# Kernel tuning notes

Measured on AMD Instinct MI355X. Metric: run time of the kernel, lower is better.

## Reference

```python
import jax, jax.numpy as jnp
import numpy as np

N_STEP = 3
N_INP = 256


def setup_inputs() -> dict:
    key = jax.random.key(0)
    ks = jax.random.split(key, 8)
    bs, L, n = 16, 128, N_INP
    s = 1.0 / np.sqrt(n)
    s2 = 1.0 / np.sqrt(2 * n)
    feat = jax.random.normal(ks[0], (bs, L, n), dtype=jnp.float32)
    mask = jnp.ones((bs, L), dtype=jnp.float32)
    # stacked per-step Linear params (torch Linear: y = x @ W.T + b)
    aggW = jax.random.uniform(ks[1], (N_STEP, n, n), minval=-s, maxval=s, dtype=jnp.float32)
    aggB = jax.random.uniform(ks[2], (N_STEP, n), minval=-s, maxval=s, dtype=jnp.float32)
    attnW = jax.random.uniform(ks[3], (N_STEP, n, 2 * n), minval=-s2, maxval=s2, dtype=jnp.float32)
    attnB = jax.random.uniform(ks[4], (N_STEP, n), minval=-s2, maxval=s2, dtype=jnp.float32)
    updW = jax.random.uniform(ks[5], (N_STEP, n, 2 * n), minval=-s2, maxval=s2, dtype=jnp.float32)
    updB = jax.random.uniform(ks[6], (N_STEP, n), minval=-s2, maxval=s2, dtype=jnp.float32)
    return {"feat": feat, "mask": mask, "aggW": aggW, "aggB": aggB,
            "attnW": attnW, "attnB": attnB, "updW": updW, "updB": updB}


def reference(feat, mask, aggW, aggB, attnW, attnB, updW, updB):
    bs, L, n = feat.shape
    hid = feat
    for i in range(N_STEP):
        hid = hid * mask[:, :, None]
        x = hid @ aggW[i].T + aggB[i]  # [b, s, n]
        # attn Linear on concat(x_s, x_j) splits into two matmuls
        W1 = attnW[i][:, :n]   # acts on x_s (sequence position)
        W2 = attnW[i][:, n:]   # acts on x_j (query node)
        p = x @ W1.T           # [b, s, n]
        q = x @ W2.T           # [b, j, n]
        # logits[b, j, s, c] = p[b, s, c] + q[b, j, c] + bias[c]
        logits = p[:, None, :, :] + q[:, :, None, :] + attnB[i]
        w = jax.nn.softmax(logits, axis=2)  # softmax over sequence dim per channel
        agg = jax.nn.sigmoid(jnp.einsum('bjsn,bsn->bjn', w, x))
        cat = jnp.concatenate([x, agg], axis=-1)  # [b, s, 2n]; dropout is identity (eval)
        hid = cat @ updW[i].T + updB[i]
    return hid
```

## Files before the change

kernel.cpp:

```cpp
#include <hip/hip_runtime.h>
#include <hip/hip_fp16.h>

#define NBLK  256
#define NPACK 192
#define NT    512
#define FPAD  16

typedef _Float16 h2_t  __attribute__((ext_vector_type(2)));
typedef _Float16 half8 __attribute__((ext_vector_type(8)));
typedef float    f32x4 __attribute__((ext_vector_type(4)));

#define AG_LD(p)    __hip_atomic_load((p), __ATOMIC_RELAXED, __HIP_MEMORY_SCOPE_AGENT)
#define AG_ST(p, v) __hip_atomic_store((p), (v), __ATOMIC_RELAXED, __HIP_MEMORY_SCOPE_AGENT)

__device__ __forceinline__ unsigned pkh(float a, float b) {
    const __half2 h = __floats2half2_rn(a, b);
    return __builtin_bit_cast(unsigned, h);
}
__device__ __forceinline__ float fdot2(unsigned w, unsigned a, float c) {
#if __has_builtin(__builtin_amdgcn_fdot2)
    return __builtin_amdgcn_fdot2(__builtin_bit_cast(h2_t, w),
                                  __builtin_bit_cast(h2_t, a), c, false);
#else
    const float2 fw = __half22float2(__builtin_bit_cast(__half2, w));
    const float2 fa = __half22float2(__builtin_bit_cast(__half2, a));
    return c + fw.x * fa.x + fw.y * fa.y;
#endif
}

__device__ __forceinline__ half8 ldw(const unsigned* p) {
    return __builtin_bit_cast(half8, *(const uint4*)p);
}
__device__ __forceinline__ f32x4 MF(half8 a, half8 b, f32x4 c) {
    return __builtin_amdgcn_mfma_f32_16x16x32_f16(a, b, c, 0, 0, 0);
}

__device__ __forceinline__ void bar_arrive(int n, unsigned* flags, int lid) {
    __syncthreads();
    if (threadIdx.x == 0)
        __hip_atomic_store(&flags[lid * FPAD], (unsigned)n, __ATOMIC_RELEASE,
                           __HIP_MEMORY_SCOPE_AGENT);
}
__device__ __forceinline__ void bar_wait_batch(int n, unsigned* flags, int b) {
    if (threadIdx.x < 16) {
        while ((int)__hip_atomic_load(&flags[(b * 16 + threadIdx.x) * FPAD],
                                      __ATOMIC_RELAXED,
                                      __HIP_MEMORY_SCOPE_AGENT) < n)
            __builtin_amdgcn_s_sleep(1);
    }
    __syncthreads();
}


__global__ __launch_bounds__(NT, 2) void pack_k(
    const float* __restrict__ aggW, const float* __restrict__ attnW,
    const float* __restrict__ updW, unsigned* __restrict__ WtH,
    unsigned* __restrict__ flags)
{
    __shared__ float Tl[64][65];
    const int bb = blockIdx.x, tid = threadIdx.x;
    const int m = bb >> 4, t = bb & 15, tr = t >> 2, tc = t & 3;
    const float* src; int stride, off;
    if (m < 3)      { src = aggW  + (size_t)m * 65536;        stride = 256; off = 0;   }
    else if (m < 6) { src = attnW + (size_t)(m - 3) * 131072; stride = 512; off = 0;   }
    else if (m < 9) { src = updW  + (size_t)(m - 6) * 131072; stride = 512; off = 0;   }
    else            { src = updW  + (size_t)(m - 9) * 131072; stride = 512; off = 256; }
    unsigned* dstu = WtH + (size_t)m * 32768;
    #pragma unroll
    for (int it = 0; it < 2; ++it) {
        const int j = it * 512 + tid, row = j >> 4, q = (j & 15) * 4;
        const float4 v = *(const float4*)(src + (size_t)(tr * 64 + row) * stride + off + tc * 64 + q);
        Tl[row][q + 0] = v.x; Tl[row][q + 1] = v.y;
        Tl[row][q + 2] = v.z; Tl[row][q + 3] = v.w;
    }
    if (bb == 0)
        for (int z = tid; z < NBLK * FPAD; z += NT) flags[z] = 0u;
    __syncthreads();
    #pragma unroll
    for (int it = 0; it < 4; ++it) {
        const int j = it * 512 + tid, cl = j >> 5, pr = j & 31;
        const unsigned val = pkh(Tl[cl][pr * 2], Tl[cl][pr * 2 + 1]);
        const int C = tr * 64 + cl, P = tc * 32 + pr;
        size_t idx;
        if (m < 9) {
            const int ttn = C >> 4, lc = C & 15;
            const int kc = P >> 4, g = (P >> 2) & 3, sl = P & 3;
            idx = (size_t)((ttn * 8 + kc) * 256 + (g * 16 + lc) * 4 + sl);
        } else {
            idx = (size_t)(P >> 2) * 1024 + (size_t)C * 4 + (P & 3);
        }
        dstu[idx] = val;
    }
}

__device__ __forceinline__ float phaseB(int i, int b, int c, int rq, int tid,
                                        const float* __restrict__ part,
                                        const unsigned* __restrict__ WtH,
                                        const float* __restrict__ updB,
                                        float* S, unsigned* aggh, uint4* buf) {
    const float* pbase = part + (size_t)((i & 1) * 256 + b * 16 + rq * 8) * 768;
    float m[8], d[8], nn[8];
    #pragma unroll
    for (int j = 0; j < 8; ++j) {
        const float* pp = pbase + (size_t)j * 768;
        m[j]  = AG_LD(pp + c);
        d[j]  = AG_LD(pp + 256 + c);
        nn[j] = AG_LD(pp + 512 + c);
    }
    #pragma unroll
    for (int st = 1; st < 8; st <<= 1) {
        #pragma unroll
        for (int j = 0; j < 8; j += 2 * st) {
            const float Mn = fmaxf(m[j], m[j + st]);
            const float sa = __expf(m[j] - Mn), sb = __expf(m[j + st] - Mn);
            d[j]  = d[j] * sa + d[j + st] * sb;
            nn[j] = nn[j] * sa + nn[j + st] * sb;
            m[j]  = Mn;
        }
    }
    S[rq * 256 + c] = m[0];
    S[512 + rq * 256 + c] = d[0];
    S[1024 + rq * 256 + c] = nn[0];
    __syncthreads();
    if (tid < 128) {
        float sg[2];
        #pragma unroll
        for (int u = 0; u < 2; ++u) {
            const int cc = 2 * tid + u;
            const float m0 = S[cc], m1 = S[256 + cc];
            const float Mx = fmaxf(m0, m1);
            const float s0 = __expf(m0 - Mx), s1 = __expf(m1 - Mx);
            const float dd = S[512 + cc] * s0 + S[768 + cc] * s1;
            const float nv = S[1024 + cc] * s0 + S[1280 + cc] * s1;
            sg[u] = 1.f / (1.f + __expf(-(nv / dd)));
        }
        aggh[tid] = pkh(sg[0], sg[1]);
    }
    __syncthreads();
    const unsigned* Uq = WtH + (size_t)(9 + i) * 32768;
    const int g0 = rq * 16;
    float a0 = 0.f, a1 = 0.f, a2 = 0.f, a3 = 0.f;
    #pragma unroll
    for (int ph = 0; ph < 2; ++ph) {
        #pragma unroll
        for (int j = 0; j < 8; ++j) {
            const uint4 w = buf[j];
            if (ph < 1)
                buf[j] = *(const uint4*)(Uq + (size_t)(g0 + 8 + j) * 1024 + c * 4);
            const uint4 a = *(const uint4*)&aggh[(g0 + ph * 8 + j) * 4];
            a0 = fdot2(w.x, a.x, a0);
            a1 = fdot2(w.y, a.y, a1);
            a2 = fdot2(w.z, a.z, a2);
            a3 = fdot2(w.w, a.w, a3);
        }
    }
    const float au = (a0 + a1) + (a2 + a3);
    S[rq * 256 + c] = au;
    __syncthreads();
    return S[c] + S[256 + c] + updB[i * 256 + c];
}

__global__ __launch_bounds__(NT, 2) void main_k(
    const float* __restrict__ feat,
    const float* __restrict__ mask,
    const float* __restrict__ aggB,
    const float* __restrict__ updB,
    const unsigned* __restrict__ WtH,
    float* __restrict__ part,
    unsigned* flags,
    float* __restrict__ out)
{
    __shared__ __align__(16) float ldsf[6152];
    unsigned* hid_uu = (unsigned*)ldsf;
    unsigned* x_uu   = (unsigned*)ldsf + 2112;
    float*    accl   = ldsf + 4224;
    float*    S      = ldsf + 4480;
    unsigned* aggh   = (unsigned*)ldsf + 6016;
    float*    msk    = ldsf + 6144;

    const int bid = blockIdx.x;
    const int tid = threadIdx.x;
    const int c   = tid & 255;
    const int rq  = tid >> 8;
    const int wid = tid >> 6, lane = tid & 63;
    const int lr  = lane & 15, lg = lane >> 4;
    const int b   = 2 * (bid & 7) + ((bid >> 3) & 1);
    const int jj  = bid >> 4;
    const int lid = b * 16 + jj;
    const int row0 = b * 128 + jj * 8;

    #pragma unroll
    for (int it = 0; it < 2; ++it) {
        const int j = it * 512 + tid, r = j >> 7, pr = j & 127;
        const float2 f = *(const float2*)(feat + (size_t)(row0 + r) * 256 + pr * 2);
        const float mv = mask[row0 + r];
        hid_uu[r * 132 + pr] = pkh(f.x * mv, f.y * mv);
    }
    for (int z = tid; z < 1056; z += NT) {
        hid_uu[1056 + z] = 0u;
        x_uu[1056 + z] = 0u;
    }
    if (tid < 8) msk[tid] = mask[row0 + tid];
    __syncthreads();

    f32x4 xu0 = {}, xu1 = {};
    uint4 u2buf[8];

    for (int i = 0; i < 3; ++i) {
        if (i > 0) {
            const float accU = phaseB(i - 1, b, c, rq, tid, part, WtH, updB,
                                      S, aggh, u2buf);
            if (rq == 0) accl[c] = accU;
            __syncthreads();
            #pragma unroll
            for (int tt = 0; tt < 2; ++tt) {
                const int t = wid * 2 + tt;
                const f32x4 xa = tt ? xu1 : xu0;
                const float av = accl[t * 16 + lr];
                float hv[4], pv[4];
                #pragma unroll
                for (int q = 0; q < 4; ++q)
                    hv[q] = (xa[q] + av) * msk[(lg & 1) * 4 + q];
                #pragma unroll
                for (int q = 0; q < 4; ++q) pv[q] = __shfl_xor(hv[q], 1);
                if (lg < 2 && !(lr & 1)) {
                    const int p2 = t * 8 + (lr >> 1);
                    #pragma unroll
                    for (int q = 0; q < 4; ++q)
                        hid_uu[(lg * 4 + q) * 132 + p2] = pkh(hv[q], pv[q]);
                }
            }
            __syncthreads();
        }

        f32x4 xr0, xr1;

        {
            const unsigned* W0 = WtH + (size_t)i * 32768;
            half8 a[8];
            #pragma unroll
            for (int kc = 0; kc < 8; ++kc)
                a[kc] = ldw(hid_uu + lr * 132 + kc * 16 + lg * 4);
            #pragma unroll
            for (int tt = 0; tt < 2; ++tt) {
                const int t = wid * 2 + tt;
                f32x4 acc = {};
                #pragma unroll
                for (int kc = 0; kc < 8; ++kc)
                    acc = MF(a[kc], ldw(W0 + (size_t)(t * 8 + kc) * 256 + lane * 4), acc);
                const float bb = aggB[i * 256 + t * 16 + lr];
                #pragma unroll
                for (int q = 0; q < 4; ++q) acc[q] += bb;
                if (tt) xr1 = acc; else xr0 = acc;
                float pv[4];
                #pragma unroll
                for (int q = 0; q < 4; ++q) pv[q] = __shfl_xor(acc[q], 1);
                if (lg < 2 && !(lr & 1)) {
                    const int p2 = t * 8 + (lr >> 1);
                    #pragma unroll
                    for (int q = 0; q < 4; ++q)
                        x_uu[(lg * 4 + q) * 132 + p2] = pkh(acc[q], pv[q]);
                }
            }
            __syncthreads();
        }

        {
            const unsigned* W1 = WtH + (size_t)(3 + i) * 32768;
            const unsigned* U1 = WtH + (size_t)(6 + i) * 32768;
            half8 a2[8];
            #pragma unroll
            for (int kc = 0; kc < 8; ++kc)
                a2[kc] = ldw(x_uu + lr * 132 + kc * 16 + lg * 4);
            float* pb = part + (size_t)((i & 1) * 256 + lid) * 768;
            #pragma unroll
            for (int tt = 0; tt < 2; ++tt) {
                const int t = wid * 2 + tt;
                f32x4 acc = {};
                #pragma unroll
                for (int kc = 0; kc < 8; ++kc)
                    acc = MF(a2[kc], ldw(W1 + (size_t)(t * 8 + kc) * 256 + lane * 4), acc);
                const f32x4 xa = tt ? xr1 : xr0;
                float m4 = fmaxf(fmaxf(acc[0], acc[1]), fmaxf(acc[2], acc[3]));
                const float m8 = fmaxf(m4, __shfl_xor(m4, 16));
                float d4 = 0.f, n4 = 0.f;
                #pragma unroll
                for (int q = 0; q < 4; ++q) {
                    const float e = __expf(acc[q] - m8);
                    d4 += e;
                    n4 += e * xa[q];
                }
                const float d8 = d4 + __shfl_xor(d4, 16);
                const float n8 = n4 + __shfl_xor(n4, 16);
                if (lg == 0) {
                    const int cc = t * 16 + lr;
                    AG_ST(pb + cc, m8);
                    AG_ST(pb + 256 + cc, d8);
                    AG_ST(pb + 512 + cc, n8);
                }
            }
            bar_arrive(i + 1, flags, lid);
            #pragma unroll
            for (int tt = 0; tt < 2; ++tt) {
                const int t = wid * 2 + tt;
                f32x4 acc = {};
                #pragma unroll
                for (int kc = 0; kc < 8; ++kc)
                    acc = MF(a2[kc], ldw(U1 + (size_t)(t * 8 + kc) * 256 + lane * 4), acc);
                if (tt) xu1 = acc; else xu0 = acc;
            }
            {
                const unsigned* Uq = WtH + (size_t)(9 + i) * 32768;
                #pragma unroll
                for (int j = 0; j < 8; ++j)
                    u2buf[j] = *(const uint4*)(Uq + (size_t)(rq * 16 + j) * 1024 + c * 4);
            }
            bar_wait_batch(i + 1, flags, b);
        }
    }

    {
        const float accU = phaseB(2, b, c, rq, tid, part, WtH, updB, S, aggh, u2buf);
        if (rq == 0) accl[c] = accU;
        __syncthreads();
        #pragma unroll
        for (int tt = 0; tt < 2; ++tt) {
            const int t = wid * 2 + tt;
            const f32x4 xa = tt ? xu1 : xu0;
            const float av = accl[t * 16 + lr];
            if (lg < 2) {
                #pragma unroll
                for (int q = 0; q < 4; ++q)
                    out[(size_t)(row0 + lg * 4 + q) * 256 + t * 16 + lr] = xa[q] + av;
            }
        }
    }
}

extern "C" void kernel_launch(void* const* d_in, const int* in_sizes, int n_in,
                              void* d_out, int out_size, void* d_ws, size_t ws_size,
                              hipStream_t stream) {
    const float* feat  = (const float*)d_in[0];
    const float* mask  = (const float*)d_in[1];
    const float* aggW  = (const float*)d_in[2];
    const float* aggB  = (const float*)d_in[3];
    const float* attnW = (const float*)d_in[4];
    const float* updW  = (const float*)d_in[6];
    const float* updB  = (const float*)d_in[7];

    unsigned* WtH = (unsigned*)d_ws;
    float* part = (float*)(WtH + 12 * 32768);
    unsigned* flags = (unsigned*)(part + 2 * 256 * 768);

    pack_k<<<NPACK, NT, 0, stream>>>(aggW, attnW, updW, WtH, flags);
    main_k<<<NBLK, NT, 0, stream>>>(feat, mask, aggB, updB, WtH, part, flags,
                                    (float*)d_out);
}
```

Before: 109.8 us.

## Software-pipeline weight fragments in registers across consecutive MFMA phases

Adds a 16-entry register buffer of weight fragments, loaded before the main loop. Each MFMA phase consumes the current buffer while prefetching the weights for the next matmul (agg to attn to upd to next step's agg), so global weight latency overlaps with compute. The kernel is also pinned to exactly two waves per EU. This costs 64 extra VGPRs per thread, which risks spills under the occupancy bound, and it issues one wasted prefetch at the last step.

Measured after the change: 115.0 us. 1.05x slower.

```diff
diff --git a/kernel.cpp b/kernel.cpp
--- a/kernel.cpp
+++ b/kernel.cpp
@@ -30,6 +30,9 @@
 
 __device__ __forceinline__ half8 ldw(const unsigned* p) {
     return __builtin_bit_cast(half8, *(const uint4*)p);
+}
+__device__ __forceinline__ half8 h8(uint4 w) {
+    return __builtin_bit_cast(half8, w);
 }
 __device__ __forceinline__ f32x4 MF(half8 a, half8 b, f32x4 c) {
     return __builtin_amdgcn_mfma_f32_16x16x32_f16(a, b, c, 0, 0, 0);
@@ -160,7 +163,9 @@
     return S[c] + S[256 + c] + updB[i * 256 + c];
 }
 
-__global__ __launch_bounds__(NT, 2) void main_k(
+__global__ __launch_bounds__(NT, 2)
+__attribute__((amdgpu_waves_per_eu(2, 2)))
+void main_k(
     const float* __restrict__ feat,
     const float* __restrict__ mask,
     const float* __restrict__ aggB,
@@ -201,6 +206,11 @@
         x_uu[1056 + z] = 0u;
     }
     if (tid < 8) msk[tid] = mask[row0 + tid];
+
+    uint4 wb[16];
+    #pragma unroll
+    for (int j = 0; j < 16; ++j)
+        wb[j] = *(const uint4*)(WtH + (size_t)(wid * 16 + j) * 256 + lane * 4);
     __syncthreads();
 
     f32x4 xu0 = {}, xu1 = {};
@@ -236,7 +246,7 @@
         f32x4 xr0, xr1;
 
         {
-            const unsigned* W0 = WtH + (size_t)i * 32768;
+            const unsigned* W1 = WtH + (size_t)(3 + i) * 32768;
             half8 a[8];
             #pragma unroll
             for (int kc = 0; kc < 8; ++kc)
@@ -246,8 +256,12 @@
                 const int t = wid * 2 + tt;
                 f32x4 acc = {};
                 #pragma unroll
-                for (int kc = 0; kc < 8; ++kc)
-                    acc = MF(a[kc], ldw(W0 + (size_t)(t * 8 + kc) * 256 + lane * 4), acc);
+                for (int kc = 0; kc < 8; ++kc) {
+                    const int j = tt * 8 + kc;
+                    const uint4 w = wb[j];
+                    wb[j] = *(const uint4*)(W1 + (size_t)(wid * 16 + j) * 256 + lane * 4);
+                    acc = MF(a[kc], h8(w), acc);
+                }
                 const float bb = aggB[i * 256 + t * 16 + lr];
                 #pragma unroll
                 for (int q = 0; q < 4; ++q) acc[q] += bb;
@@ -266,8 +280,8 @@
         }
 
         {
-            const unsigned* W1 = WtH + (size_t)(3 + i) * 32768;
             const unsigned* U1 = WtH + (size_t)(6 + i) * 32768;
+            const unsigned* Wn = WtH + (size_t)(i == 2 ? 0 : i + 1) * 32768;
             half8 a2[8];
             #pragma unroll
             for (int kc = 0; kc < 8; ++kc)
@@ -278,8 +292,12 @@
                 const int t = wid * 2 + tt;
                 f32x4 acc = {};
                 #pragma unroll
-                for (int kc = 0; kc < 8; ++kc)
-                    acc = MF(a2[kc], ldw(W1 + (size_t)(t * 8 + kc) * 256 + lane * 4), acc);
+                for (int kc = 0; kc < 8; ++kc) {
+                    const int j = tt * 8 + kc;
+                    const uint4 w = wb[j];
+                    wb[j] = *(const uint4*)(U1 + (size_t)(wid * 16 + j) * 256 + lane * 4);
+                    acc = MF(a2[kc], h8(w), acc);
+                }
                 const f32x4 xa = tt ? xr1 : xr0;
                 float m4 = fmaxf(fmaxf(acc[0], acc[1]), fmaxf(acc[2], acc[3]));
                 const float m8 = fmaxf(m4, __shfl_xor(m4, 16));
@@ -302,11 +320,14 @@
             bar_arrive(i + 1, flags, lid);
             #pragma unroll
             for (int tt = 0; tt < 2; ++tt) {
-                const int t = wid * 2 + tt;
                 f32x4 acc = {};
                 #pragma unroll
-                for (int kc = 0; kc < 8; ++kc)
-                    acc = MF(a2[kc], ldw(U1 + (size_t)(t * 8 + kc) * 256 + lane * 4), acc);
+                for (int kc = 0; kc < 8; ++kc) {
+                    const int j = tt * 8 + kc;
+                    const uint4 w = wb[j];
+                    wb[j] = *(const uint4*)(Wn + (size_t)(wid * 16 + j) * 256 + lane * 4);
+                    acc = MF(a2[kc], h8(w), acc);
+                }
                 if (tt) xu1 = acc; else xu0 = acc;
             }
             {
```

## Halve block count so each block owns 16 rows, filling MFMA tiles

Applied to the files above, without the earlier changes.

Cuts the persistent grid from 256 to 128 blocks, and each block now processes 16 sequence rows instead of 8. The 16x16 MFMA tiles were previously half padding with zeros; now every row is real work. The softmax partials are reduced across 16 rows with an extra shuffle, and the cross-block merge and barrier wait shrink from 16 to 8 partners per batch. In exchange, only half as many CUs are active, and each block loads the same weights for twice the rows.

Result: faster. 105.0 us (-4.4%).

```diff
diff --git a/kernel.cpp b/kernel.cpp
--- a/kernel.cpp
+++ b/kernel.cpp
@@ -1,7 +1,7 @@
 #include <hip/hip_runtime.h>
 #include <hip/hip_fp16.h>
 
-#define NBLK  256
+#define NBLK  128
 #define NPACK 192
 #define NT    512
 #define FPAD  16
@@ -42,8 +42,8 @@
                            __HIP_MEMORY_SCOPE_AGENT);
 }
 __device__ __forceinline__ void bar_wait_batch(int n, unsigned* flags, int b) {
-    if (threadIdx.x < 16) {
-        while ((int)__hip_atomic_load(&flags[(b * 16 + threadIdx.x) * FPAD],
+    if (threadIdx.x < 8) {
+        while ((int)__hip_atomic_load(&flags[(b * 8 + threadIdx.x) * FPAD],
                                       __ATOMIC_RELAXED,
                                       __HIP_MEMORY_SCOPE_AGENT) < n)
             __builtin_amdgcn_s_sleep(1);
@@ -74,7 +74,7 @@
         Tl[row][q + 2] = v.z; Tl[row][q + 3] = v.w;
     }
     if (bb == 0)
-        for (int z = tid; z < NBLK * FPAD; z += NT) flags[z] = 0u;
+        for (int z = tid; z < 256 * FPAD; z += NT) flags[z] = 0u;
     __syncthreads();
     #pragma unroll
     for (int it = 0; it < 4; ++it) {
@@ -98,19 +98,19 @@
                                         const unsigned* __restrict__ WtH,
                                         const float* __restrict__ updB,
                                         float* S, unsigned* aggh, uint4* buf) {
-    const float* pbase = part + (size_t)((i & 1) * 256 + b * 16 + rq * 8) * 768;
-    float m[8], d[8], nn[8];
-    #pragma unroll
-    for (int j = 0; j < 8; ++j) {
+    const float* pbase = part + (size_t)((i & 1) * 128 + b * 8 + rq * 4) * 768;
+    float m[4], d[4], nn[4];
+    #pragma unroll
+    for (int j = 0; j < 4; ++j) {
         const float* pp = pbase + (size_t)j * 768;
         m[j]  = AG_LD(pp + c);
         d[j]  = AG_LD(pp + 256 + c);
         nn[j] = AG_LD(pp + 512 + c);
     }
     #pragma unroll
-    for (int st = 1; st < 8; st <<= 1) {
+    for (int st = 1; st < 4; st <<= 1) {
         #pragma unroll
-        for (int j = 0; j < 8; j += 2 * st) {
+        for (int j = 0; j < 4; j += 2 * st) {
             const float Mn = fmaxf(m[j], m[j + st]);
             const float sa = __expf(m[j] - Mn), sb = __expf(m[j + st] - Mn);
             d[j]  = d[j] * sa + d[j + st] * sb;
@@ -170,7 +170,7 @@
     unsigned* flags,
     float* __restrict__ out)
 {
-    __shared__ __align__(16) float ldsf[6152];
+    __shared__ __align__(16) float ldsf[6160];
     unsigned* hid_uu = (unsigned*)ldsf;
     unsigned* x_uu   = (unsigned*)ldsf + 2112;
     float*    accl   = ldsf + 4224;
@@ -186,22 +186,20 @@
     const int lr  = lane & 15, lg = lane >> 4;
     const int b   = 2 * (bid & 7) + ((bid >> 3) & 1);
     const int jj  = bid >> 4;
-    const int lid = b * 16 + jj;
-    const int row0 = b * 128 + jj * 8;
-
-    #pragma unroll
-    for (int it = 0; it < 2; ++it) {
+    const int lid = b * 8 + jj;
+    const int row0 = b * 128 + jj * 16;
+
+    #pragma unroll
+    for (int it = 0; it < 4; ++it) {
         const int j = it * 512 + tid, r = j >> 7, pr = j & 127;
         const float2 f = *(const float2*)(feat + (size_t)(row0 + r) * 256 + pr * 2);
         const float mv = mask[row0 + r];
         hid_uu[r * 132 + pr] = pkh(f.x * mv, f.y * mv);
     }
-    for (int z = tid; z < 1056; z += NT) {
-        hid_uu[1056 + z] = 0u;
-        x_uu[1056 + z] = 0u;
-    }
-    if (tid < 8) msk[tid] = mask[row0 + tid];
-    __syncthreads();
+    if (tid < 16) msk[tid] = mask[row0 + tid];
+    __syncthreads();
+
+    const int ct0 = wid * 2, ct1 = wid * 2 + 1;
 
     f32x4 xu0 = {}, xu1 = {};
     uint4 u2buf[8];
@@ -220,10 +218,10 @@
                 float hv[4], pv[4];
                 #pragma unroll
                 for (int q = 0; q < 4; ++q)
-                    hv[q] = (xa[q] + av) * msk[(lg & 1) * 4 + q];
+                    hv[q] = (xa[q] + av) * msk[lg * 4 + q];
                 #pragma unroll
                 for (int q = 0; q < 4; ++q) pv[q] = __shfl_xor(hv[q], 1);
-                if (lg < 2 && !(lr & 1)) {
+                if (!(lr & 1)) {
                     const int p2 = t * 8 + (lr >> 1);
                     #pragma unroll
                     for (int q = 0; q < 4; ++q)
@@ -255,7 +253,7 @@
                 float pv[4];
                 #pragma unroll
                 for (int q = 0; q < 4; ++q) pv[q] = __shfl_xor(acc[q], 1);
-                if (lg < 2 && !(lr & 1)) {
+                if (!(lr & 1)) {
                     const int p2 = t * 8 + (lr >> 1);
                     #pragma unroll
                     for (int q = 0; q < 4; ++q)
@@ -272,7 +270,7 @@
             #pragma unroll
             for (int kc = 0; kc < 8; ++kc)
                 a2[kc] = ldw(x_uu + lr * 132 + kc * 16 + lg * 4);
-            float* pb = part + (size_t)((i & 1) * 256 + lid) * 768;
+            float* pb = part + (size_t)((i & 1) * 128 + lid) * 768;
             #pragma unroll
             for (int tt = 0; tt < 2; ++tt) {
                 const int t = wid * 2 + tt;
@@ -282,21 +280,22 @@
                     acc = MF(a2[kc], ldw(W1 + (size_t)(t * 8 + kc) * 256 + lane * 4), acc);
                 const f32x4 xa = tt ? xr1 : xr0;
                 float m4 = fmaxf(fmaxf(acc[0], acc[1]), fmaxf(acc[2], acc[3]));
-                const float m8 = fmaxf(m4, __shfl_xor(m4, 16));
+                m4 = fmaxf(m4, __shfl_xor(m4, 16));
+                const float m16 = fmaxf(m4, __shfl_xor(m4, 32));
                 float d4 = 0.f, n4 = 0.f;
                 #pragma unroll
                 for (int q = 0; q < 4; ++q) {
-                    const float e = __expf(acc[q] - m8);
+                    const float e = __expf(acc[q] - m16);
                     d4 += e;
                     n4 += e * xa[q];
                 }
-                const float d8 = d4 + __shfl_xor(d4, 16);
-                const float n8 = n4 + __shfl_xor(n4, 16);
+                d4 += __shfl_xor(d4, 16); d4 += __shfl_xor(d4, 32);
+                n4 += __shfl_xor(n4, 16); n4 += __shfl_xor(n4, 32);
                 if (lg == 0) {
                     const int cc = t * 16 + lr;
-                    AG_ST(pb + cc, m8);
-                    AG_ST(pb + 256 + cc, d8);
-                    AG_ST(pb + 512 + cc, n8);
+                    AG_ST(pb + cc, m16);
+                    AG_ST(pb + 256 + cc, d4);
+                    AG_ST(pb + 512 + cc, n4);
                 }
             }
             bar_arrive(i + 1, flags, lid);
@@ -328,11 +327,9 @@
             const int t = wid * 2 + tt;
             const f32x4 xa = tt ? xu1 : xu0;
             const float av = accl[t * 16 + lr];
-            if (lg < 2) {
-                #pragma unroll
-                for (int q = 0; q < 4; ++q)
-                    out[(size_t)(row0 + lg * 4 + q) * 256 + t * 16 + lr] = xa[q] + av;
-            }
+            #pragma unroll
+            for (int q = 0; q < 4; ++q)
+                out[(size_t)(row0 + lg * 4 + q) * 256 + t * 16 + lr] = xa[q] + av;
         }
     }
 }
```
